# Kernel optimization log

Measured on AMD Instinct MI355X. Metric: run time of the kernel, lower is better.

The kernel has to match this reference:

```python
import jax, jax.numpy as jnp
import numpy as np

N = 4096        # num nodes
D = 512         # d_model (in_dim)
F = 512         # dff (out_dim)
H = 4           # num_heads
ALPHA = 0.3     # tf.keras LeakyReLU default


def setup_inputs() -> dict:
    key = jax.random.key(0)
    ks = jax.random.split(key, 9)
    s_in = 1.0 / np.sqrt(D)
    s_out = 1.0 / np.sqrt(F)
    return {
        "nodes": jax.random.normal(ks[0], (N, D), jnp.float32),
        "edges": jax.random.normal(ks[1], (N, D), jnp.float32),
        "labels": jax.random.normal(ks[2], (N, D), jnp.float32),
        # edge_layer Dense(dff)
        "We": jax.random.normal(ks[3], (D, F), jnp.float32) * s_in,
        "be": jnp.zeros((F,), jnp.float32),
        # per-head kernels stacked on leading head axis
        "W": jax.random.normal(ks[4], (H, D, F), jnp.float32) * s_in,
        "b": jax.random.normal(ks[5], (H, F), jnp.float32) * 0.01,
        "u": jax.random.normal(ks[6], (H, F), jnp.float32) * s_out,  # attn_kernel_self (squeezed)
        "v": jax.random.normal(ks[7], (H, F), jnp.float32) * s_out,  # attn_kernel_neighs (squeezed)
    }


def reference(nodes, edges, labels, We, be, W, b, u, v):
    # edge projection shared across heads: Dense(edges + labels)
    e = (edges + labels) @ We + be                       # [N, F]
    # per-head node projection: features = nodes @ W_h + b_h
    feats = jnp.einsum('nd,hdf->hnf', nodes, W) + b[:, None, :]   # [H, N, F]
    # rank-1 additive attention scores
    a_self = jnp.einsum('hnf,hf->hn', feats, u)          # [H, N]
    a_neigh = jnp.einsum('hnf,hf->hn', feats, v)         # [H, N]
    feats = feats + e[None]                              # [H, N, F]
    scores = a_self[:, :, None] * a_neigh[:, None, :]    # [H, N, N] outer product
    scores = jnp.where(scores >= 0, scores, ALPHA * scores)  # LeakyReLU(0.3)
    attn = jax.nn.softmax(scores, axis=-1)               # [H, N, N]
    out = jnp.einsum('hnm,hmf->hnf', attn, feats)        # [H, N, F]
    return jax.nn.relu(out.mean(axis=0))                 # [N, F]
```

## Files before the change

### kernel.cpp

```cpp
#include <hip/hip_runtime.h>

#define NN 4096
#define DD 512
#define FF 512
#define HH 4
#define KK 1024

typedef _Float16 f16;
typedef f16 f16x8 __attribute__((ext_vector_type(8)));
typedef f16 f16x4 __attribute__((ext_vector_type(4)));
typedef float f32x4 __attribute__((ext_vector_type(4)));

typedef __attribute__((address_space(1))) void gvoid;
typedef __attribute__((address_space(3))) void svoid;
__device__ __forceinline__ void glds16(const void* g, void* s) {
    __builtin_amdgcn_global_load_lds((gvoid*)g, (svoid*)s, 16, 0, 0);
}

__device__ __attribute__((aligned(16))) f16 g_catA[NN * KK];
__device__ __attribute__((aligned(16))) f16 g_catB[HH * FF * KK];
__device__ __attribute__((aligned(16))) f16 g_featsH[HH * FF * NN];
__device__ __attribute__((aligned(16))) f16 g_oaccH[(size_t)2 * HH * NN * FF];
__device__ float g_Zp[2 * HH * NN];
__device__ float g_bcat[HH * FF];
__device__ float g_tu[HH * DD], g_tv[HH * DD], g_bu[HH], g_bv[HH];
__device__ float g_p[HH * NN], g_q[HH * NN], g_M[HH * NN];

#define PREP_CONV 4104
#define PREP_TRAN 320
#define PREP_UV   513

__global__ __launch_bounds__(256) void k_prep(const float* __restrict__ nodes, const float* __restrict__ edges,
                                              const float* __restrict__ labels, const float* __restrict__ We,
                                              const float* __restrict__ W, const float* __restrict__ be,
                                              const float* __restrict__ b, const float* __restrict__ u,
                                              const float* __restrict__ v) {
    __shared__ float lds[64 * 65];
    int bx = blockIdx.x;
    int tid = threadIdx.x;
    if (bx < PREP_CONV) {
        int id = bx * 256 + tid;
        const int NQ = NN * DD / 4;
        if (id < NQ) {
            f32x4 vv = *(const f32x4*)(nodes + (size_t)id * 4);
            f16x4 ov;
#pragma unroll
            for (int k = 0; k < 4; ++k) ov[k] = (f16)vv[k];
            *(f16x4*)&g_catA[(size_t)(id >> 7) * KK + (id & 127) * 4] = ov;
            return;
        }
        id -= NQ;
        if (id < NQ) {
            f32x4 ev = *(const f32x4*)(edges  + (size_t)id * 4);
            f32x4 lv = *(const f32x4*)(labels + (size_t)id * 4);
            f16x4 ov;
#pragma unroll
            for (int k = 0; k < 4; ++k) ov[k] = (f16)(ev[k] + lv[k]);
            *(f16x4*)&g_catA[(size_t)(id >> 7) * KK + 512 + (id & 127) * 4] = ov;
            return;
        }
        id -= NQ;
        if (id < HH * FF) { g_bcat[id] = b[id] + be[id & 511]; return; }
        return;
    }
    if (bx < PREP_CONV + PREP_TRAN) {
        int bid = bx - PREP_CONV;
        int mi = bid >> 6;
        int t64 = bid & 63;
        const float* src = (mi == 0) ? We : (W + (size_t)(mi - 1) * DD * FF);
        int ti = t64 >> 3, tj = t64 & 7;
        int r = tid >> 2, cseg = (tid & 3) * 16;
#pragma unroll
        for (int kq = 0; kq < 4; ++kq) {
            f32x4 vv = *(const f32x4*)(src + (size_t)(ti * 64 + r) * 512 + tj * 64 + cseg + kq * 4);
            *(f32x4*)&lds[r * 65 + cseg + kq * 4] = vv;
        }
        __syncthreads();
        int fl = tid >> 2, dseg = (tid & 3) * 16;
        f16x8 o0, o1;
#pragma unroll
        for (int k = 0; k < 8; ++k) o0[k] = (f16)lds[(dseg + k) * 65 + fl];
#pragma unroll
        for (int k = 0; k < 8; ++k) o1[k] = (f16)lds[(dseg + 8 + k) * 65 + fl];
        size_t frow = (size_t)(tj * 64 + fl);
        size_t dcol = (size_t)(ti * 64 + dseg);
        if (mi == 0) {
#pragma unroll
            for (int hh = 0; hh < HH; ++hh) {
                size_t ob = ((size_t)hh * FF + frow) * KK + 512 + dcol;
                *(f16x8*)&g_catB[ob] = o0;
                *(f16x8*)&g_catB[ob + 8] = o1;
            }
        } else {
            size_t ob = ((size_t)(mi - 1) * FF + frow) * KK + dcol;
            *(f16x8*)&g_catB[ob] = o0;
            *(f16x8*)&g_catB[ob + 8] = o1;
        }
        return;
    }
    {
        int row = (bx - PREP_CONV - PREP_TRAN) * 4 + (tid >> 6);
        int lane = tid & 63;
        float su = 0.f, sv = 0.f;
        if (row < HH * DD) {
            int h = row >> 9, d = row & 511;
            size_t wb = (size_t)h * DD * FF + (size_t)d * FF;
#pragma unroll
            for (int j = 0; j < 8; ++j) {
                int f = lane + 64 * j;
                float wv = W[wb + f];
                su += wv * u[(size_t)h * FF + f];
                sv += wv * v[(size_t)h * FF + f];
            }
        } else if (row < HH * DD + HH) {
            int h = row - HH * DD;
#pragma unroll
            for (int j = 0; j < 8; ++j) {
                int f = lane + 64 * j;
                float bvv = b[(size_t)h * FF + f];
                su += bvv * u[(size_t)h * FF + f];
                sv += bvv * v[(size_t)h * FF + f];
            }
        }
#pragma unroll
        for (int m = 1; m < 64; m <<= 1) {
            su += __shfl_xor(su, m, 64);
            sv += __shfl_xor(sv, m, 64);
        }
        if (lane == 0 && row < HH * DD + HH) {
            if (row < HH * DD) { g_tu[row] = su; g_tv[row] = sv; }
            else { g_bu[row - HH * DD] = su; g_bv[row - HH * DD] = sv; }
        }
    }
}

__global__ __launch_bounds__(256) void k_pq() {
    int row = blockIdx.x * 4 + (threadIdx.x >> 6);
    int lane = threadIdx.x & 63;
    int h = row >> 12, n = row & 4095;
    const f16* nb = g_catA + (size_t)n * KK + lane * 8;
    const float* tu = g_tu + h * DD + lane * 8;
    const float* tv = g_tv + h * DD + lane * 8;
    f16x8 nv8 = *(const f16x8*)nb;
    f32x4 tu0 = *(const f32x4*)tu, tu1 = *(const f32x4*)(tu + 4);
    f32x4 tv0 = *(const f32x4*)tv, tv1 = *(const f32x4*)(tv + 4);
    float pa = 0.f, qa = 0.f;
#pragma unroll
    for (int j = 0; j < 4; ++j) {
        float nv = (float)nv8[j];
        pa += nv * tu0[j];
        qa += nv * tv0[j];
    }
#pragma unroll
    for (int j = 0; j < 4; ++j) {
        float nv = (float)nv8[4 + j];
        pa += nv * tu1[j];
        qa += nv * tv1[j];
    }
#pragma unroll
    for (int m = 1; m < 64; m <<= 1) {
        pa += __shfl_xor(pa, m, 64);
        qa += __shfl_xor(qa, m, 64);
    }
    if (lane == 0) {
        g_p[row] = pa + g_bu[h];
        g_q[row] = qa + g_bv[h];
    }
}

__global__ __launch_bounds__(256, 2) void k_gemm_feats() {
    __shared__ f16 As[128 * 128];
    __shared__ f16 Bs[128 * 128];
    int tid = threadIdx.x;
    int lane = tid & 63, wave = tid >> 6;
    int wr = wave & 1, wc = wave >> 1;
    int c = lane & 15, g = lane >> 4;
    int n0 = blockIdx.x * 128, f0 = blockIdx.y * 128;
    int h = blockIdx.z;
    const f16* Bgl = g_catB + (size_t)h * FF * KK;
    int r4 = lane >> 4;
    int ch = lane & 15;
    f32x4 acc[4][4] = {};
    for (int kk = 0; kk < KK; kk += 128) {
        __syncthreads();
#pragma unroll
        for (int j = 0; j < 8; ++j) {
            int rowb = wave * 32 + j * 4;
            int row = rowb + r4;
            int src = (ch ^ (row & 15)) * 8;
            glds16(g_catA + (size_t)(n0 + row) * KK + kk + src, &As[rowb * 128]);
            glds16(Bgl    + (size_t)(f0 + row) * KK + kk + src, &Bs[rowb * 128]);
        }
        __syncthreads();
#pragma unroll
        for (int s = 0; s < 4; ++s) {
            f16x8 af[4], bf[4];
#pragma unroll
            for (int i = 0; i < 4; ++i) {
                int ra = wr * 64 + i * 16 + c;
                af[i] = *(const f16x8*)&As[ra * 128 + (((s * 4 + g) ^ (ra & 15)) * 8)];
            }
#pragma unroll
            for (int jj = 0; jj < 4; ++jj) {
                int rb = wc * 64 + jj * 16 + c;
                bf[jj] = *(const f16x8*)&Bs[rb * 128 + (((s * 4 + g) ^ (rb & 15)) * 8)];
            }
#pragma unroll
            for (int i = 0; i < 4; ++i)
#pragma unroll
                for (int jj = 0; jj < 4; ++jj)
                    acc[i][jj] = __builtin_amdgcn_mfma_f32_16x16x32_f16(af[i], bf[jj], acc[i][jj], 0, 0, 0);
        }
    }
#pragma unroll
    for (int jj = 0; jj < 4; ++jj) {
        int f = f0 + wc * 64 + jj * 16 + c;
        float bv = g_bcat[h * FF + f];
#pragma unroll
        for (int i = 0; i < 4; ++i) {
            int r0 = n0 + wr * 64 + i * 16 + g * 4;
            f16x4 ov;
#pragma unroll
            for (int rr = 0; rr < 4; ++rr) ov[rr] = (f16)(acc[i][jj][rr] + bv);
            *(f16x4*)(g_featsH + ((size_t)h * FF + f) * NN + r0) = ov;
        }
    }
}

__global__ __launch_bounds__(256) void k_mstat() {
    __shared__ float red[256];
    int h = blockIdx.x;
    int tid = threadIdx.x;
    float lmax = -1e30f, lmin = 1e30f;
    for (int i = tid; i < NN; i += 256) {
        float qv = g_q[h * NN + i];
        lmax = fmaxf(lmax, qv);
        lmin = fminf(lmin, qv);
    }
    red[tid] = lmax;
    __syncthreads();
    for (int s = 128; s > 0; s >>= 1) {
        if (tid < s) red[tid] = fmaxf(red[tid], red[tid + s]);
        __syncthreads();
    }
    float qmax = red[0];
    __syncthreads();
    red[tid] = lmin;
    __syncthreads();
    for (int s = 128; s > 0; s >>= 1) {
        if (tid < s) red[tid] = fminf(red[tid], red[tid + s]);
        __syncthreads();
    }
    float qmin = red[0];
#pragma unroll
    for (int j = 0; j < 16; ++j) {
        int n = tid + j * 256;
        float pv = g_p[h * NN + n];
        float se = pv * (pv >= 0.f ? qmax : qmin);
        g_M[h * NN + n] = fmaxf(se, 0.3f * se);
    }
}

#define WCALC(qv, dstvec, idx)                                              \
    {                                                                       \
        float s_ = pv * (qv);                                               \
        s_ = fmaxf(s_, 0.3f * s_);                                          \
        float e_ = __builtin_amdgcn_exp2f(__builtin_fmaf(s_, L2E, -mvb));   \
        zacc += e_;                                                         \
        dstvec[idx] = (f16)e_;                                              \
    }
#define GEN16(q0, q1, q2, q3, w0, w1)                                       \
    {                                                                       \
        _Pragma("unroll") for (int k_ = 0; k_ < 4; ++k_) {                  \
            WCALC((q0)[k_], w0, k_);                                        \
            WCALC((q1)[k_], w0, 4 + k_);                                    \
            WCALC((q2)[k_], w1, k_);                                        \
            WCALC((q3)[k_], w1, 4 + k_);                                    \
        }                                                                   \
    }

__global__ __launch_bounds__(512, 2) void k_gemm_out() {
    __shared__ f16 As2[2][128 * 64];
    __shared__ f16 BsL[2][512 * 32];
    __shared__ f16 BsH[2][512 * 32];
    int tid = threadIdx.x;
    int lane = tid & 63, wave = tid >> 6;
    int wr = wave & 1;
    int wf = wave >> 1;
    int c = lane & 15, g = lane >> 4;
    int n0 = blockIdx.x * 128;
    int h = blockIdx.y;
    int ks = blockIdx.z;
    int wn = tid >> 2, kq = (tid & 3) * 16;
    const float L2E = 1.44269504f;
    float pv = g_p[h * NN + n0 + wn];
    float mvb = g_M[h * NN + n0 + wn] * L2E + 6.0f;
    const float* qh = g_q + h * NN + ks * 2048;
    const f16* Bgl = g_featsH + (size_t)h * FF * NN + (size_t)ks * 2048;
    int brow = lane >> 2;
    int bksw = ((lane & 3) ^ (brow & 3)) * 8;
    int aw0 = wn * 64 + (((tid & 3) * 2 + 0) ^ (wn & 7)) * 8;
    int aw1 = wn * 64 + (((tid & 3) * 2 + 1) ^ (wn & 7)) * 8;
    float zacc = 0.f;
    f32x4 acc[4][8] = {};
    f16x8 wA, wB;

    {
        const float* qp = qh + kq;
        f32x4 q0 = *(const f32x4*)qp, q1 = *(const f32x4*)(qp + 4),
              q2 = *(const f32x4*)(qp + 8), q3 = *(const f32x4*)(qp + 12);
        GEN16(q0, q1, q2, q3, wA, wB);
        *(f16x8*)&As2[0][aw0] = wA;
        *(f16x8*)&As2[0][aw1] = wB;
#pragma unroll
        for (int j = 0; j < 4; ++j) {
            int frow = wave * 64 + j * 16;
            glds16(Bgl + (size_t)(frow + brow) * NN + bksw,      &BsL[0][frow * 32]);
            glds16(Bgl + (size_t)(frow + brow) * NN + 32 + bksw, &BsH[0][frow * 32]);
        }
        const float* qp1 = qh + 64 + kq;
        q0 = *(const f32x4*)qp1; q1 = *(const f32x4*)(qp1 + 4);
        q2 = *(const f32x4*)(qp1 + 8); q3 = *(const f32x4*)(qp1 + 12);
        GEN16(q0, q1, q2, q3, wA, wB);
    }
    __syncthreads();

    int cur = 0;
    for (int t = 0; t < 32; ++t) {
        f32x4 q0, q1, q2, q3;
        if (t < 30) {
            const float* qp = qh + t * 64 + 128 + kq;
            q0 = *(const f32x4*)qp; q1 = *(const f32x4*)(qp + 4);
            q2 = *(const f32x4*)(qp + 8); q3 = *(const f32x4*)(qp + 12);
        }
        if (t < 31) {
            int nxt = cur ^ 1;
            int kk2 = t * 64 + 64;
#pragma unroll
            for (int j = 0; j < 4; ++j) {
                int frow = wave * 64 + j * 16;
                glds16(Bgl + (size_t)(frow + brow) * NN + kk2 + bksw,      &BsL[nxt][frow * 32]);
                glds16(Bgl + (size_t)(frow + brow) * NN + kk2 + 32 + bksw, &BsH[nxt][frow * 32]);
            }
            *(f16x8*)&As2[nxt][aw0] = wA;
            *(f16x8*)&As2[nxt][aw1] = wB;
        }
        {
            f16x8 af[4], bfr[8];
#pragma unroll
            for (int i = 0; i < 4; ++i) {
                int ra = wr * 64 + i * 16 + c;
                af[i] = *(const f16x8*)&As2[cur][ra * 64 + ((g ^ (ra & 7)) * 8)];
            }
#pragma unroll
            for (int jj = 0; jj < 8; ++jj)
                bfr[jj] = *(const f16x8*)&BsL[cur][(wf * 128 + jj * 16 + c) * 32 + ((g ^ (c & 3)) * 8)];
#pragma unroll
            for (int i = 0; i < 4; ++i)
#pragma unroll
                for (int jj = 0; jj < 8; ++jj)
                    acc[i][jj] = __builtin_amdgcn_mfma_f32_16x16x32_f16(af[i], bfr[jj], acc[i][jj], 0, 0, 0);
        }
        if (t < 30) GEN16(q0, q1, q2, q3, wA, wB);
        {
            f16x8 af[4], bfr[8];
#pragma unroll
            for (int i = 0; i < 4; ++i) {
                int ra = wr * 64 + i * 16 + c;
                af[i] = *(const f16x8*)&As2[cur][ra * 64 + (((4 + g) ^ (ra & 7)) * 8)];
            }
#pragma unroll
            for (int jj = 0; jj < 8; ++jj)
                bfr[jj] = *(const f16x8*)&BsH[cur][(wf * 128 + jj * 16 + c) * 32 + ((g ^ (c & 3)) * 8)];
#pragma unroll
            for (int i = 0; i < 4; ++i)
#pragma unroll
                for (int jj = 0; jj < 8; ++jj)
                    acc[i][jj] = __builtin_amdgcn_mfma_f32_16x16x32_f16(af[i], bfr[jj], acc[i][jj], 0, 0, 0);
        }
        __syncthreads();
        cur ^= 1;
    }
    zacc += __shfl_xor(zacc, 1, 64);
    zacc += __shfl_xor(zacc, 2, 64);
    if ((tid & 3) == 0) g_Zp[(size_t)(h * 2 + ks) * NN + n0 + wn] = zacc;
    f16* O = g_oaccH + (size_t)(h * 2 + ks) * NN * FF;
#pragma unroll
    for (int jj = 0; jj < 8; ++jj) {
        int f = wf * 128 + jj * 16 + c;
#pragma unroll
        for (int i = 0; i < 4; ++i) {
            int r0 = n0 + wr * 64 + i * 16 + g * 4;
#pragma unroll
            for (int rr = 0; rr < 4; ++rr)
                O[(size_t)(r0 + rr) * FF + f] = (f16)acc[i][jj][rr];
        }
    }
}

__global__ void k_reduce(float* __restrict__ out) {
    int t = blockIdx.x * 256 + threadIdx.x;
    size_t i = (size_t)t * 4;
    int n = t >> 7;
    const size_t NF = (size_t)NN * FF;
    f32x4 s = {0.f, 0.f, 0.f, 0.f};
#pragma unroll
    for (int h = 0; h < HH; ++h) {
        float Z = g_Zp[(size_t)(2 * h) * NN + n] + g_Zp[(size_t)(2 * h + 1) * NN + n];
        float sc = 0.25f / Z;
        f16x4 a = *(const f16x4*)(g_oaccH + (size_t)(2 * h) * NF + i);
        f16x4 bsl = *(const f16x4*)(g_oaccH + (size_t)(2 * h + 1) * NF + i);
#pragma unroll
        for (int rr = 0; rr < 4; ++rr) s[rr] += ((float)a[rr] + (float)bsl[rr]) * sc;
    }
    f32x4 o;
#pragma unroll
    for (int rr = 0; rr < 4; ++rr) o[rr] = fmaxf(s[rr], 0.f);
    *(f32x4*)(out + i) = o;
}

extern "C" void kernel_launch(void* const* d_in, const int* in_sizes, int n_in,
                              void* d_out, int out_size, void* d_ws, size_t ws_size,
                              hipStream_t stream) {
    (void)in_sizes; (void)n_in; (void)out_size; (void)d_ws; (void)ws_size;
    const float* nodes  = (const float*)d_in[0];
    const float* edges  = (const float*)d_in[1];
    const float* labels = (const float*)d_in[2];
    const float* We     = (const float*)d_in[3];
    const float* be     = (const float*)d_in[4];
    const float* W      = (const float*)d_in[5];
    const float* b      = (const float*)d_in[6];
    const float* u      = (const float*)d_in[7];
    const float* v      = (const float*)d_in[8];

    k_prep<<<PREP_CONV + PREP_TRAN + PREP_UV, 256, 0, stream>>>(nodes, edges, labels, We, W, be, b, u, v);
    k_pq<<<4096, 256, 0, stream>>>();
    k_gemm_feats<<<dim3(32, 4, 4), 256, 0, stream>>>();
    k_mstat<<<HH, 256, 0, stream>>>();
    k_gemm_out<<<dim3(32, 4, 2), 512, 0, stream>>>();
    k_reduce<<<2048, 256, 0, stream>>>((float*)d_out);
}
```

Baseline: 230.2 us.

## Split attention-output GEMM loop into four barrier-delimited phases with priority bumps

Splits each K-step of the output GEMM into four sub-phases of 16 MFMAs. Each phase is bracketed by workgroup barriers and s_setprio so waves interleave LDS reads and exp-weight generation with MFMA bursts, in the style of ping-pong scheduling. Exp-weight generation is spread across the phases, and explicit waitcnt plus s_barrier replace __syncthreads. This adds four barriers per iteration and relies on manual waitcnt correctness, so it risks extra synchronisation stalls.

```diff
diff --git a/kernel.cpp b/kernel.cpp
--- a/kernel.cpp
+++ b/kernel.cpp
@@ -278,6 +278,20 @@
             WCALC((q3)[k_], w1, 4 + k_);                                    \
         }                                                                   \
     }
+#define GEN4(qv, w, base)                                                   \
+    {                                                                       \
+        _Pragma("unroll") for (int k_ = 0; k_ < 4; ++k_) {                  \
+            WCALC((qv)[k_], w, (base) + k_);                                \
+        }                                                                   \
+    }
+#define PHASE_OPEN()                                                        \
+    __builtin_amdgcn_s_barrier();                                           \
+    asm volatile("s_waitcnt lgkmcnt(0)" ::: "memory");                      \
+    __builtin_amdgcn_sched_barrier(0);                                      \
+    __builtin_amdgcn_s_setprio(1);
+#define PHASE_CLOSE()                                                       \
+    __builtin_amdgcn_s_setprio(0);                                          \
+    __builtin_amdgcn_s_barrier();
 
 __global__ __launch_bounds__(512, 2) void k_gemm_out() {
     __shared__ f16 As2[2][128 * 64];
@@ -323,7 +337,8 @@
         q2 = *(const f32x4*)(qp1 + 8); q3 = *(const f32x4*)(qp1 + 12);
         GEN16(q0, q1, q2, q3, wA, wB);
     }
-    __syncthreads();
+    asm volatile("s_waitcnt vmcnt(0) lgkmcnt(0)" ::: "memory");
+    __builtin_amdgcn_s_barrier();
 
     int cur = 0;
     for (int t = 0; t < 32; ++t) {
@@ -345,40 +360,74 @@
             *(f16x8*)&As2[nxt][aw0] = wA;
             *(f16x8*)&As2[nxt][aw1] = wB;
         }
+        f16x8 af[4];
         {
-            f16x8 af[4], bfr[8];
+            f16x8 bfr[4];
 #pragma unroll
             for (int i = 0; i < 4; ++i) {
                 int ra = wr * 64 + i * 16 + c;
                 af[i] = *(const f16x8*)&As2[cur][ra * 64 + ((g ^ (ra & 7)) * 8)];
             }
 #pragma unroll
-            for (int jj = 0; jj < 8; ++jj)
+            for (int jj = 0; jj < 4; ++jj)
                 bfr[jj] = *(const f16x8*)&BsL[cur][(wf * 128 + jj * 16 + c) * 32 + ((g ^ (c & 3)) * 8)];
+            PHASE_OPEN();
 #pragma unroll
             for (int i = 0; i < 4; ++i)
 #pragma unroll
-                for (int jj = 0; jj < 8; ++jj)
+                for (int jj = 0; jj < 4; ++jj)
                     acc[i][jj] = __builtin_amdgcn_mfma_f32_16x16x32_f16(af[i], bfr[jj], acc[i][jj], 0, 0, 0);
-        }
-        if (t < 30) GEN16(q0, q1, q2, q3, wA, wB);
+            PHASE_CLOSE();
+        }
         {
-            f16x8 af[4], bfr[8];
+            f16x8 bfr[4];
+#pragma unroll
+            for (int jj = 0; jj < 4; ++jj)
+                bfr[jj] = *(const f16x8*)&BsL[cur][(wf * 128 + (jj + 4) * 16 + c) * 32 + ((g ^ (c & 3)) * 8)];
+            if (t < 30) GEN4(q0, wA, 0);
+            PHASE_OPEN();
+#pragma unroll
+            for (int i = 0; i < 4; ++i)
+#pragma unroll
+                for (int jj = 0; jj < 4; ++jj)
+                    acc[i][jj + 4] = __builtin_amdgcn_mfma_f32_16x16x32_f16(af[i], bfr[jj], acc[i][jj + 4], 0, 0, 0);
+            PHASE_CLOSE();
+        }
+        {
+            f16x8 bfr[4];
 #pragma unroll
             for (int i = 0; i < 4; ++i) {
                 int ra = wr * 64 + i * 16 + c;
                 af[i] = *(const f16x8*)&As2[cur][ra * 64 + (((4 + g) ^ (ra & 7)) * 8)];
             }
 #pragma unroll
-            for (int jj = 0; jj < 8; ++jj)
+            for (int jj = 0; jj < 4; ++jj)
                 bfr[jj] = *(const f16x8*)&BsH[cur][(wf * 128 + jj * 16 + c) * 32 + ((g ^ (c & 3)) * 8)];
+            if (t < 30) GEN4(q1, wA, 4);
+            PHASE_OPEN();
 #pragma unroll
             for (int i = 0; i < 4; ++i)
 #pragma unroll
-                for (int jj = 0; jj < 8; ++jj)
+                for (int jj = 0; jj < 4; ++jj)
                     acc[i][jj] = __builtin_amdgcn_mfma_f32_16x16x32_f16(af[i], bfr[jj], acc[i][jj], 0, 0, 0);
-        }
-        __syncthreads();
+            PHASE_CLOSE();
+        }
+        {
+            f16x8 bfr[4];
+#pragma unroll
+            for (int jj = 0; jj < 4; ++jj)
+                bfr[jj] = *(const f16x8*)&BsH[cur][(wf * 128 + (jj + 4) * 16 + c) * 32 + ((g ^ (c & 3)) * 8)];
+            if (t < 30) { GEN4(q2, wB, 0); GEN4(q3, wB, 4); }
+            PHASE_OPEN();
+#pragma unroll
+            for (int i = 0; i < 4; ++i)
+#pragma unroll
+                for (int jj = 0; jj < 4; ++jj)
+                    acc[i][jj + 4] = __builtin_amdgcn_mfma_f32_16x16x32_f16(af[i], bfr[jj], acc[i][jj + 4], 0, 0, 0);
+            __builtin_amdgcn_s_setprio(0);
+            asm volatile("s_waitcnt vmcnt(0) lgkmcnt(0)" ::: "memory");
+            __builtin_amdgcn_s_barrier();
+        }
         cur ^= 1;
     }
     zacc += __shfl_xor(zacc, 1, 64);
```

After: 249.7 us. 1.08x slower.

## Switch attention GEMM to 32x32x16 MFMA with unified swizzled B tile

Applied to the files above, without the earlier changes.

Rewrites the main k_gemm_out inner loop to use 32x32x16 f16 MFMA tiles in place of 16x16x32. The two half-K B buffers are merged into a single 64-wide XOR-swizzled LDS tile, which changes both the staging and fragment addressing. Exponent-weight generation is now interleaved between MFMA k-steps to hide its latency. The larger MFMA reduces LDS fragment loads per FLOP, at the cost of a new accumulator layout that the store epilogue must follow. k_reduce is also widened to process 8 elements per thread.

```diff
diff --git a/kernel.cpp b/kernel.cpp
--- a/kernel.cpp
+++ b/kernel.cpp
@@ -10,6 +10,7 @@
 typedef f16 f16x8 __attribute__((ext_vector_type(8)));
 typedef f16 f16x4 __attribute__((ext_vector_type(4)));
 typedef float f32x4 __attribute__((ext_vector_type(4)));
+typedef float f32x16 __attribute__((ext_vector_type(16)));
 
 typedef __attribute__((address_space(1))) void gvoid;
 typedef __attribute__((address_space(3))) void svoid;
@@ -269,25 +270,30 @@
         zacc += e_;                                                         \
         dstvec[idx] = (f16)e_;                                              \
     }
-#define GEN16(q0, q1, q2, q3, w0, w1)                                       \
+#define GEN8(qa, qb, w)                                                     \
     {                                                                       \
         _Pragma("unroll") for (int k_ = 0; k_ < 4; ++k_) {                  \
-            WCALC((q0)[k_], w0, k_);                                        \
-            WCALC((q1)[k_], w0, 4 + k_);                                    \
-            WCALC((q2)[k_], w1, k_);                                        \
-            WCALC((q3)[k_], w1, 4 + k_);                                    \
+            WCALC((qa)[k_], w, k_);                                         \
+            WCALC((qb)[k_], w, 4 + k_);                                     \
+        }                                                                   \
+    }
+#define STAGE_B(buf, kkoff)                                                 \
+    {                                                                       \
+        _Pragma("unroll") for (int j = 0; j < 8; ++j) {                     \
+            int row_ = wave * 64 + j * 8 + r8;                              \
+            glds16(Bgl + (size_t)row_ * NN + (kkoff) + ((ch ^ (row_ & 7)) * 8), \
+                   &Bs[buf][(wave * 64 + j * 8) * 64]);                     \
         }                                                                   \
     }
 
 __global__ __launch_bounds__(512, 2) void k_gemm_out() {
     __shared__ f16 As2[2][128 * 64];
-    __shared__ f16 BsL[2][512 * 32];
-    __shared__ f16 BsH[2][512 * 32];
+    __shared__ f16 Bs[2][512 * 64];
     int tid = threadIdx.x;
     int lane = tid & 63, wave = tid >> 6;
     int wr = wave & 1;
     int wf = wave >> 1;
-    int c = lane & 15, g = lane >> 4;
+    int c5 = lane & 31, h5 = lane >> 5;
     int n0 = blockIdx.x * 128;
     int h = blockIdx.y;
     int ks = blockIdx.z;
@@ -297,31 +303,30 @@
     float mvb = g_M[h * NN + n0 + wn] * L2E + 6.0f;
     const float* qh = g_q + h * NN + ks * 2048;
     const f16* Bgl = g_featsH + (size_t)h * FF * NN + (size_t)ks * 2048;
-    int brow = lane >> 2;
-    int bksw = ((lane & 3) ^ (brow & 3)) * 8;
+    int r8 = lane >> 3, ch = lane & 7;
     int aw0 = wn * 64 + (((tid & 3) * 2 + 0) ^ (wn & 7)) * 8;
     int aw1 = wn * 64 + (((tid & 3) * 2 + 1) ^ (wn & 7)) * 8;
+    int arow = (wr * 64 + c5) * 64;
+    int brow = (wf * 128 + c5) * 64;
+    int csw = (c5 & 7);
     float zacc = 0.f;
-    f32x4 acc[4][8] = {};
+    f32x16 acc[2][4] = {};
     f16x8 wA, wB;
 
     {
         const float* qp = qh + kq;
         f32x4 q0 = *(const f32x4*)qp, q1 = *(const f32x4*)(qp + 4),
               q2 = *(const f32x4*)(qp + 8), q3 = *(const f32x4*)(qp + 12);
-        GEN16(q0, q1, q2, q3, wA, wB);
+        GEN8(q0, q1, wA);
+        GEN8(q2, q3, wB);
         *(f16x8*)&As2[0][aw0] = wA;
         *(f16x8*)&As2[0][aw1] = wB;
-#pragma unroll
-        for (int j = 0; j < 4; ++j) {
-            int frow = wave * 64 + j * 16;
-            glds16(Bgl + (size_t)(frow + brow) * NN + bksw,      &BsL[0][frow * 32]);
-            glds16(Bgl + (size_t)(frow + brow) * NN + 32 + bksw, &BsH[0][frow * 32]);
-        }
+        STAGE_B(0, 0);
         const float* qp1 = qh + 64 + kq;
         q0 = *(const f32x4*)qp1; q1 = *(const f32x4*)(qp1 + 4);
         q2 = *(const f32x4*)(qp1 + 8); q3 = *(const f32x4*)(qp1 + 12);
-        GEN16(q0, q1, q2, q3, wA, wB);
+        GEN8(q0, q1, wA);
+        GEN8(q2, q3, wB);
     }
     __syncthreads();
 
@@ -336,47 +341,31 @@
         if (t < 31) {
             int nxt = cur ^ 1;
             int kk2 = t * 64 + 64;
-#pragma unroll
-            for (int j = 0; j < 4; ++j) {
-                int frow = wave * 64 + j * 16;
-                glds16(Bgl + (size_t)(frow + brow) * NN + kk2 + bksw,      &BsL[nxt][frow * 32]);
-                glds16(Bgl + (size_t)(frow + brow) * NN + kk2 + 32 + bksw, &BsH[nxt][frow * 32]);
-            }
+            STAGE_B(nxt, kk2);
             *(f16x8*)&As2[nxt][aw0] = wA;
             *(f16x8*)&As2[nxt][aw1] = wB;
         }
-        {
-            f16x8 af[4], bfr[8];
-#pragma unroll
-            for (int i = 0; i < 4; ++i) {
-                int ra = wr * 64 + i * 16 + c;
-                af[i] = *(const f16x8*)&As2[cur][ra * 64 + ((g ^ (ra & 7)) * 8)];
-            }
-#pragma unroll
-            for (int jj = 0; jj < 8; ++jj)
-                bfr[jj] = *(const f16x8*)&BsL[cur][(wf * 128 + jj * 16 + c) * 32 + ((g ^ (c & 3)) * 8)];
-#pragma unroll
-            for (int i = 0; i < 4; ++i)
-#pragma unroll
-                for (int jj = 0; jj < 8; ++jj)
-                    acc[i][jj] = __builtin_amdgcn_mfma_f32_16x16x32_f16(af[i], bfr[jj], acc[i][jj], 0, 0, 0);
-        }
-        if (t < 30) GEN16(q0, q1, q2, q3, wA, wB);
-        {
-            f16x8 af[4], bfr[8];
-#pragma unroll
-            for (int i = 0; i < 4; ++i) {
-                int ra = wr * 64 + i * 16 + c;
-                af[i] = *(const f16x8*)&As2[cur][ra * 64 + (((4 + g) ^ (ra & 7)) * 8)];
-            }
-#pragma unroll
-            for (int jj = 0; jj < 8; ++jj)
-                bfr[jj] = *(const f16x8*)&BsH[cur][(wf * 128 + jj * 16 + c) * 32 + ((g ^ (c & 3)) * 8)];
-#pragma unroll
-            for (int i = 0; i < 4; ++i)
-#pragma unroll
-                for (int jj = 0; jj < 8; ++jj)
-                    acc[i][jj] = __builtin_amdgcn_mfma_f32_16x16x32_f16(af[i], bfr[jj], acc[i][jj], 0, 0, 0);
+#pragma unroll
+        for (int sk = 0; sk < 4; ++sk) {
+            int cph = ((sk * 2 + h5) ^ csw) * 8;
+            f16x8 af0 = *(const f16x8*)&As2[cur][arow + cph];
+            f16x8 af1 = *(const f16x8*)&As2[cur][arow + 2048 + cph];
+            f16x8 bf0 = *(const f16x8*)&Bs[cur][brow + cph];
+            f16x8 bf1 = *(const f16x8*)&Bs[cur][brow + 2048 + cph];
+            f16x8 bf2 = *(const f16x8*)&Bs[cur][brow + 4096 + cph];
+            f16x8 bf3 = *(const f16x8*)&Bs[cur][brow + 6144 + cph];
+            acc[0][0] = __builtin_amdgcn_mfma_f32_32x32x16_f16(af0, bf0, acc[0][0], 0, 0, 0);
+            acc[0][1] = __builtin_amdgcn_mfma_f32_32x32x16_f16(af0, bf1, acc[0][1], 0, 0, 0);
+            acc[0][2] = __builtin_amdgcn_mfma_f32_32x32x16_f16(af0, bf2, acc[0][2], 0, 0, 0);
+            acc[0][3] = __builtin_amdgcn_mfma_f32_32x32x16_f16(af0, bf3, acc[0][3], 0, 0, 0);
+            acc[1][0] = __builtin_amdgcn_mfma_f32_32x32x16_f16(af1, bf0, acc[1][0], 0, 0, 0);
+            acc[1][1] = __builtin_amdgcn_mfma_f32_32x32x16_f16(af1, bf1, acc[1][1], 0, 0, 0);
+            acc[1][2] = __builtin_amdgcn_mfma_f32_32x32x16_f16(af1, bf2, acc[1][2], 0, 0, 0);
+            acc[1][3] = __builtin_amdgcn_mfma_f32_32x32x16_f16(af1, bf3, acc[1][3], 0, 0, 0);
+            if (t < 30) {
+                if (sk == 1) GEN8(q0, q1, wA);
+                if (sk == 2) GEN8(q2, q3, wB);
+            }
         }
         __syncthreads();
         cur ^= 1;
@@ -386,37 +375,42 @@
     if ((tid & 3) == 0) g_Zp[(size_t)(h * 2 + ks) * NN + n0 + wn] = zacc;
     f16* O = g_oaccH + (size_t)(h * 2 + ks) * NN * FF;
 #pragma unroll
-    for (int jj = 0; jj < 8; ++jj) {
-        int f = wf * 128 + jj * 16 + c;
-#pragma unroll
-        for (int i = 0; i < 4; ++i) {
-            int r0 = n0 + wr * 64 + i * 16 + g * 4;
-#pragma unroll
-            for (int rr = 0; rr < 4; ++rr)
-                O[(size_t)(r0 + rr) * FF + f] = (f16)acc[i][jj][rr];
-        }
-    }
+    for (int it = 0; it < 2; ++it)
+#pragma unroll
+        for (int jt = 0; jt < 4; ++jt) {
+            int f = wf * 128 + jt * 32 + c5;
+#pragma unroll
+            for (int q = 0; q < 4; ++q) {
+                int r0 = n0 + wr * 64 + it * 32 + q * 8 + h5 * 4;
+#pragma unroll
+                for (int rr = 0; rr < 4; ++rr)
+                    O[(size_t)(r0 + rr) * FF + f] = (f16)acc[it][jt][q * 4 + rr];
+            }
+        }
 }
 
 __global__ void k_reduce(float* __restrict__ out) {
     int t = blockIdx.x * 256 + threadIdx.x;
-    size_t i = (size_t)t * 4;
-    int n = t >> 7;
+    size_t i = (size_t)t * 8;
+    int n = t >> 6;
     const size_t NF = (size_t)NN * FF;
-    f32x4 s = {0.f, 0.f, 0.f, 0.f};
+    float s[8] = {0.f, 0.f, 0.f, 0.f, 0.f, 0.f, 0.f, 0.f};
 #pragma unroll
     for (int h = 0; h < HH; ++h) {
         float Z = g_Zp[(size_t)(2 * h) * NN + n] + g_Zp[(size_t)(2 * h + 1) * NN + n];
         float sc = 0.25f / Z;
-        f16x4 a = *(const f16x4*)(g_oaccH + (size_t)(2 * h) * NF + i);
-        f16x4 bsl = *(const f16x4*)(g_oaccH + (size_t)(2 * h + 1) * NF + i);
-#pragma unroll
-        for (int rr = 0; rr < 4; ++rr) s[rr] += ((float)a[rr] + (float)bsl[rr]) * sc;
-    }
-    f32x4 o;
-#pragma unroll
-    for (int rr = 0; rr < 4; ++rr) o[rr] = fmaxf(s[rr], 0.f);
-    *(f32x4*)(out + i) = o;
+        f16x8 a = *(const f16x8*)(g_oaccH + (size_t)(2 * h) * NF + i);
+        f16x8 bsl = *(const f16x8*)(g_oaccH + (size_t)(2 * h + 1) * NF + i);
+#pragma unroll
+        for (int rr = 0; rr < 8; ++rr) s[rr] += ((float)a[rr] + (float)bsl[rr]) * sc;
+    }
+    f32x4 o0, o1;
+#pragma unroll
+    for (int rr = 0; rr < 4; ++rr) o0[rr] = fmaxf(s[rr], 0.f);
+#pragma unroll
+    for (int rr = 0; rr < 4; ++rr) o1[rr] = fmaxf(s[4 + rr], 0.f);
+    *(f32x4*)(out + i) = o0;
+    *(f32x4*)(out + i + 4) = o1;
 }
 
 extern "C" void kernel_launch(void* const* d_in, const int* in_sizes, int n_in,
@@ -438,5 +432,5 @@
     k_gemm_feats<<<dim3(32, 4, 4), 256, 0, stream>>>();
     k_mstat<<<HH, 256, 0, stream>>>();
     k_gemm_out<<<dim3(32, 4, 2), 512, 0, stream>>>();
-    k_reduce<<<2048, 256, 0, stream>>>((float*)d_out);
-}
+    k_reduce<<<1024, 256, 0, stream>>>((float*)d_out);
+}
```

New measurement: 223.6 us. 2.9% less time.
